# Kernel tuning notes

Hardware: AMD Instinct MI355X
Metric: run time of the kernel (lower is better)

The kernel has to match this reference:

```python
import jax, jax.numpy as jnp
import numpy as np

NODE_DIM = 256
EDGE_DIM = 128
NODE_IN = 768 + 769 + 4 + 1 + 3  # 1545


def setup_inputs() -> dict:
    key = jax.random.key(0)
    ks = jax.random.split(key, 16)
    B, N, H, W, C = 8, 128, 128, 128, 768
    obj_feats = jax.random.normal(ks[0], (B, N, 769), dtype=jnp.float32)
    masks = jax.random.uniform(ks[1], (B, N, H, W), dtype=jnp.float32)
    features = jax.random.normal(ks[2], (B, C, H, W), dtype=jnp.float32)
    bboxes = jax.random.uniform(ks[3], (B, N, 4), dtype=jnp.float32)
    conf = jax.random.uniform(ks[4], (B, N), dtype=jnp.float32)
    depth = jax.random.uniform(ks[5], (B, 1, H, W), dtype=jnp.float32) + 0.1
    # near-identity pose so homogeneous divide is well-conditioned
    pose = jnp.eye(4, dtype=jnp.float32)[None] + 0.01 * jax.random.normal(ks[6], (B, 4, 4), dtype=jnp.float32)
    s = 0.02
    node_w1 = s * jax.random.normal(ks[7], (512, NODE_IN), dtype=jnp.float32)
    node_b1 = jnp.zeros((512,), dtype=jnp.float32)
    node_w2 = s * jax.random.normal(ks[8], (NODE_DIM, 512), dtype=jnp.float32)
    node_b2 = jnp.zeros((NODE_DIM,), dtype=jnp.float32)
    edge_w1 = s * jax.random.normal(ks[9], (256, 2 * NODE_DIM), dtype=jnp.float32)
    edge_b1 = jnp.zeros((256,), dtype=jnp.float32)
    edge_w2 = s * jax.random.normal(ks[10], (EDGE_DIM, 256), dtype=jnp.float32)
    edge_b2 = jnp.zeros((EDGE_DIM,), dtype=jnp.float32)
    return dict(obj_feats=obj_feats, masks=masks, features=features, bboxes=bboxes,
                conf=conf, depth=depth, pose=pose,
                node_w1=node_w1, node_b1=node_b1, node_w2=node_w2, node_b2=node_b2,
                edge_w1=edge_w1, edge_b1=edge_b1, edge_w2=edge_w2, edge_b2=edge_b2)


def _forward(obj_feats, masks, features, bboxes, conf, depth, pose,
             node_w1, node_b1, node_w2, node_b2,
             edge_w1, edge_b1, edge_w2, edge_b2):
    B, C, H, W = features.shape
    N = masks.shape[1]
    K = jnp.eye(3, dtype=features.dtype)  # self.intrinsics

    # --- mask pooling: normalized mask-weighted average of features ---
    feats_flat = features.reshape(B, C, H * W)                 # [B,C,HW]
    m_flat = masks.reshape(B, N, H * W)                        # [B,N,HW]
    m_norm = m_flat / (m_flat.sum(-1, keepdims=True) + 1e-6)
    pooled = jnp.einsum('bnh,bch->bnc', m_norm, feats_flat)    # [B,N,C]

    # --- positional encoding ---
    x1, y1, x2, y2 = bboxes[..., 0], bboxes[..., 1], bboxes[..., 2], bboxes[..., 3]
    pos_feat = jnp.stack([(x1 + x2) / 2, (y1 + y2) / 2, x2 - x1, y2 - y1], axis=-1)  # [B,N,4]

    # --- motion prior ---
    ys = jnp.arange(H, dtype=masks.dtype)
    xs = jnp.arange(W, dtype=masks.dtype)
    mask_sum = masks.sum((-1, -2)) + 1e-6                      # [B,N]
    cx = jnp.einsum('bnhw,w->bn', masks, xs) / mask_sum
    cy = jnp.einsum('bnhw,h->bn', masks, ys) / mask_sum
    cx_idx = jnp.clip(jnp.round(cx).astype(jnp.int32), 0, W - 1)
    cy_idx = jnp.clip(jnp.round(cy).astype(jnp.int32), 0, H - 1)
    b_idx = jnp.arange(B)[:, None]                             # [B,1]
    z = depth[b_idx, 0, cy_idx, cx_idx]                        # [B,N]
    X = (cx - K[0, 2]) * z / K[0, 0]
    Y = (cy - K[1, 2]) * z / K[1, 1]
    ones = jnp.ones_like(z)
    P_h = jnp.stack([X, Y, z, ones], axis=-1)                  # [B,N,4]
    P_next = jnp.einsum('bij,bnj->bni', pose, P_h)             # [B,N,4]
    motion = P_next[..., :3] / P_next[..., 3:]                 # [B,N,3]

    # --- node MLP ---
    node_input = jnp.concatenate([pooled, obj_feats, pos_feat, conf[..., None], motion], axis=-1)
    h = jax.nn.relu(node_input @ node_w1.T + node_b1)
    node_emb = h @ node_w2.T + node_b2                         # [B,N,node_dim]

    # --- edge MLP: cat([n_i, n_j]) @ W1 == n_i @ W1a + n_j @ W1b (avoid O(N^2 * 2D) cat) ---
    D = node_emb.shape[-1]
    w1a, w1b = edge_w1[:, :D], edge_w1[:, D:]
    hi = node_emb @ w1a.T                                      # [B,N,256]
    hj = node_emb @ w1b.T                                      # [B,N,256]
    he = jax.nn.relu(hi[:, :, None, :] + hj[:, None, :, :] + edge_b1)  # [B,N,N,256]
    edge_emb = he @ edge_w2.T + edge_b2                        # [B,N,N,edge_dim]

    # --- adjacency: exp(-cdist) ---
    sq = jnp.sum(node_emb * node_emb, axis=-1)                 # [B,N]
    d2 = sq[:, :, None] + sq[:, None, :] - 2.0 * jnp.einsum('bnd,bmd->bnm', node_emb, node_emb)
    d2 = jnp.maximum(d2, 0.0)
    d = jnp.where(d2 > 0, jnp.sqrt(jnp.where(d2 > 0, d2, 1.0)), 0.0)  # grad-safe sqrt at 0
    adj = jnp.exp(-d)
    return node_emb, edge_emb, adj


def reference(obj_feats, masks, features, bboxes, conf, depth, pose,
              node_w1, node_b1, node_w2, node_b2,
              edge_w1, edge_b1, edge_w2, edge_b2):
    return _forward(obj_feats, masks, features, bboxes, conf, depth, pose,
                    node_w1, node_b1, node_w2, node_b2,
                    edge_w1, edge_b1, edge_w2, edge_b2)
```

## Files before the change

kernel.cpp:

```cpp
#include <hip/hip_runtime.h>
#include <hip/hip_bf16.h>

#define B_   8
#define N_   128
#define HW_  16384
#define C_   768
#define NIN_ 1545
#define NINP_ 1600
#define D1_  512
#define D_   256
#define EO_  128
#define KC_  8
#define CT_  12

typedef short s16x8 __attribute__((ext_vector_type(8)));
typedef float f32x16 __attribute__((ext_vector_type(16)));

__device__ __forceinline__ unsigned short f2bf(float x) {
  union { __hip_bfloat16 h; unsigned short u; } cv;
  cv.h = __float2bfloat16(x);
  return cv.u;
}

__global__ __launch_bounds__(256) void prep_k(const float* __restrict__ masks,
                                              const float* __restrict__ depth,
                                              const float* __restrict__ pose,
                                              float4* __restrict__ stats,
                                              unsigned short* __restrict__ masks_bf,
                                              const float* __restrict__ w1,
                                              const float* __restrict__ w2,
                                              const float* __restrict__ ew1,
                                              const float* __restrict__ ew2,
                                              unsigned short* __restrict__ w1b,
                                              unsigned short* __restrict__ w2b,
                                              unsigned short* __restrict__ we1b,
                                              unsigned short* __restrict__ ew2b) {
  if (blockIdx.x >= 1024) {
    int i = (blockIdx.x - 1024) * 256 + threadIdx.x;
    if (i < 512 * NINP_) {
      int r = i / NINP_, k = i - r * NINP_;
      w1b[i] = f2bf(k < NIN_ ? w1[r * NIN_ + k] : 0.0f);
      return;
    }
    i -= 512 * NINP_;
    if (i < 256 * 512) { w2b[i] = f2bf(w2[i]); return; }
    i -= 256 * 512;
    if (i < 512 * 256) {
      int r = i >> 8, k = i & 255;
      we1b[i] = f2bf(r < 256 ? ew1[r * 512 + k] : ew1[(r - 256) * 512 + 256 + k]);
      return;
    }
    i -= 512 * 256;
    if (i < 128 * 256) { ew2b[i] = f2bf(ew2[i]); }
    return;
  }
  int row = blockIdx.x;
  int b = row >> 7;
  const float4* mp = (const float4*)(masks + (size_t)row * HW_);
  unsigned short* mo = masks_bf + (size_t)row * HW_;
  double s = 0.0, sx = 0.0, sy = 0.0;
  for (int it = 0; it < 16; ++it) {
    int i4 = threadIdx.x + it * 256;
    float4 v = mp[i4];
    ushort4 pv = { f2bf(v.x), f2bf(v.y), f2bf(v.z), f2bf(v.w) };
    *(ushort4*)(mo + i4 * 4) = pv;
    int flat = i4 * 4;
    int y = flat >> 7, xb = flat & 127;
    double rs = (double)v.x + (double)v.y + (double)v.z + (double)v.w;
    s += rs;
    sx += (double)v.x * xb + (double)v.y * (xb + 1) + (double)v.z * (xb + 2) + (double)v.w * (xb + 3);
    sy += rs * (double)y;
  }
  for (int off = 32; off; off >>= 1) {
    s  += __shfl_down(s,  off);
    sx += __shfl_down(sx, off);
    sy += __shfl_down(sy, off);
  }
  __shared__ double red[3][4];
  int w = threadIdx.x >> 6, l = threadIdx.x & 63;
  if (l == 0) { red[0][w] = s; red[1][w] = sx; red[2][w] = sy; }
  __syncthreads();
  if (threadIdx.x == 0) {
    s  = red[0][0] + red[0][1] + red[0][2] + red[0][3];
    sx = red[1][0] + red[1][1] + red[1][2] + red[1][3];
    sy = red[2][0] + red[2][1] + red[2][2] + red[2][3];
    double msum = s + 1e-6;
    double cx = sx / msum, cy = sy / msum;
    int cxi = (int)rint(cx); cxi = min(127, max(0, cxi));
    int cyi = (int)rint(cy); cyi = min(127, max(0, cyi));
    double z = (double)depth[(size_t)b * HW_ + cyi * 128 + cxi];
    double Ph[4] = { cx * z, cy * z, z, 1.0 };
    const float* P = pose + b * 16;
    double pn[4];
    #pragma unroll
    for (int r = 0; r < 4; ++r)
      pn[r] = (double)P[r*4+0]*Ph[0] + (double)P[r*4+1]*Ph[1] + (double)P[r*4+2]*Ph[2] + (double)P[r*4+3]*Ph[3];
    double inv3 = 1.0 / pn[3];
    stats[row] = make_float4((float)(1.0 / msum), (float)(pn[0]*inv3), (float)(pn[1]*inv3), (float)(pn[2]*inv3));
  }
}

__global__ __launch_bounds__(256) void pooled_k(const unsigned short* __restrict__ masks_bf,
                                                const float* __restrict__ feats,
                                                float* __restrict__ Spart) {
  __shared__ short As[128 * 72];
  __shared__ short Bs[64 * 72];
  int id = blockIdx.x;
  int b  = id / 96;
  int lx = id - b * 96;
  int ct = lx % 12, kc = lx / 12;
  const unsigned short* mb = masks_bf + (size_t)b * N_ * HW_;
  const float* fb = feats + ((size_t)b * C_ + (size_t)ct * 64) * HW_;
  int t = threadIdx.x, w = t >> 6, l = t & 63;
  int rsel = l & 31, khalf = l >> 5;
  f32x16 acc[2];
  #pragma unroll
  for (int nt = 0; nt < 2; ++nt)
    #pragma unroll
    for (int i = 0; i < 16; ++i) acc[nt][i] = 0.0f;

  for (int kt = 0; kt < 32; ++kt) {
    int kbase = kc * 2048 + kt * 64;
    #pragma unroll
    for (int c = 0; c < 4; ++c) {
      int chunk = t + 256 * c;
      int row = chunk >> 3;
      int kof = (chunk & 7) * 8;
      *(uint4*)((unsigned short*)As + row * 72 + kof) =
          *(const uint4*)(mb + (size_t)row * HW_ + kbase + kof);
    }
    #pragma unroll
    for (int c = 0; c < 4; ++c) {
      int chunk = t + 256 * c;
      int row = chunk >> 4;
      int kof = (chunk & 15) << 2;
      float4 vb = *(const float4*)(fb + (size_t)row * HW_ + kbase + kof);
      ushort4 pb = { f2bf(vb.x), f2bf(vb.y), f2bf(vb.z), f2bf(vb.w) };
      *(ushort4*)((unsigned short*)Bs + row * 72 + kof) = pb;
    }
    __syncthreads();
    #pragma unroll
    for (int ks = 0; ks < 4; ++ks) {
      s16x8 a = *(const s16x8*)&As[(w * 32 + rsel) * 72 + ks * 16 + khalf * 8];
      #pragma unroll
      for (int nt = 0; nt < 2; ++nt) {
        s16x8 bf = *(const s16x8*)&Bs[(nt * 32 + rsel) * 72 + ks * 16 + khalf * 8];
        acc[nt] = __builtin_amdgcn_mfma_f32_32x32x16_bf16(a, bf, acc[nt], 0, 0, 0);
      }
    }
    __syncthreads();
  }
  float* op = Spart + (size_t)kc * 786432 + (size_t)b * 98304;
  #pragma unroll
  for (int nt = 0; nt < 2; ++nt)
    #pragma unroll
    for (int reg = 0; reg < 16; ++reg) {
      int rm = w * 32 + (reg & 3) + 8 * (reg >> 2) + 4 * khalf;
      int cn = ct * 64 + nt * 32 + rsel;
      op[rm * C_ + cn] = acc[nt][reg];
    }
}

__global__ __launch_bounds__(256) void assemble_k(const float* __restrict__ Spart,
                                                  const float4* __restrict__ stats,
                                                  const float* __restrict__ obj,
                                                  const float* __restrict__ bboxes,
                                                  const float* __restrict__ conf,
                                                  unsigned short* __restrict__ ni) {
  int r = blockIdx.x;
  float4 st = stats[r];
  float x1 = bboxes[r*4+0], y1 = bboxes[r*4+1], x2 = bboxes[r*4+2], y2 = bboxes[r*4+3];
  for (int k = threadIdx.x; k < NINP_; k += 256) {
    float v;
    if (k < 768) {
      float acc = 0.0f;
      #pragma unroll
      for (int kc = 0; kc < KC_; ++kc) acc += Spart[(size_t)kc * 786432 + (size_t)r * C_ + k];
      v = acc * st.x;
    } else if (k < 1537) v = obj[(size_t)r * 769 + (k - 768)];
    else if (k == 1537) v = 0.5f * (x1 + x2);
    else if (k == 1538) v = 0.5f * (y1 + y2);
    else if (k == 1539) v = x2 - x1;
    else if (k == 1540) v = y2 - y1;
    else if (k == 1541) v = conf[r];
    else if (k == 1542) v = st.y;
    else if (k == 1543) v = st.z;
    else if (k == 1544) v = st.w;
    else v = 0.0f;
    ni[(size_t)r * NINP_ + k] = f2bf(v);
  }
}

template <bool RELU, bool BIAS, int OUTM>
__global__ __launch_bounds__(256) void gemm64_k(const unsigned short* __restrict__ A,
                                                const unsigned short* __restrict__ Bm,
                                                const float* __restrict__ bias,
                                                float* __restrict__ Cf,
                                                unsigned short* __restrict__ Cb,
                                                int K, int N) {
  __shared__ short As[64 * 72];
  __shared__ short Bs[64 * 72];
  int n0 = blockIdx.x * 64, m0 = blockIdx.y * 64;
  int t = threadIdx.x, w = t >> 6, l = t & 63;
  int rsel = l & 31, khalf = l >> 5;
  int mh = (w & 1) * 32, nh = (w >> 1) * 32;
  f32x16 acc;
  #pragma unroll
  for (int i = 0; i < 16; ++i) acc[i] = 0.0f;

  for (int k0 = 0; k0 < K; k0 += 64) {
    #pragma unroll
    for (int c = 0; c < 2; ++c) {
      int chunk = t + 256 * c;
      int row = chunk >> 3, kof = (chunk & 7) * 8;
      *(uint4*)((unsigned short*)As + row * 72 + kof) =
          *(const uint4*)&A[(size_t)(m0 + row) * K + k0 + kof];
      *(uint4*)((unsigned short*)Bs + row * 72 + kof) =
          *(const uint4*)&Bm[(size_t)(n0 + row) * K + k0 + kof];
    }
    __syncthreads();
    #pragma unroll
    for (int ks = 0; ks < 4; ++ks) {
      s16x8 a = *(const s16x8*)&As[(mh + rsel) * 72 + ks * 16 + khalf * 8];
      s16x8 bf = *(const s16x8*)&Bs[(nh + rsel) * 72 + ks * 16 + khalf * 8];
      acc = __builtin_amdgcn_mfma_f32_32x32x16_bf16(a, bf, acc, 0, 0, 0);
    }
    __syncthreads();
  }
  #pragma unroll
  for (int reg = 0; reg < 16; ++reg) {
    int rm = m0 + mh + (reg & 3) + 8 * (reg >> 2) + 4 * khalf;
    int cn = n0 + nh + rsel;
    float v = acc[reg];
    if (BIAS) v += bias[cn];
    if (RELU) v = fmaxf(v, 0.0f);
    if (OUTM == 0 || OUTM == 2) Cf[(size_t)rm * N + cn] = v;
    if (OUTM == 1 || OUTM == 2) Cb[(size_t)rm * N + cn] = f2bf(v);
  }
}

__global__ __launch_bounds__(256) void edge_adj_k(const float* __restrict__ hihj,
                                                  const unsigned short* __restrict__ ew2b,
                                                  const float* __restrict__ eb1,
                                                  const float* __restrict__ eb2,
                                                  const float* __restrict__ ne,
                                                  float* __restrict__ out_edge,
                                                  float* __restrict__ out_adj) {
  __shared__ union {
    struct { short W2s[128 * 264]; float hi_s[256]; float b1_s[256]; float b2_s[128]; } e;
    struct { float njs[128 * 65]; float nei[256]; float red[3][256]; } a;
  } sm;
  int id = blockIdx.x;
  int lg = (id & 7) * 256 + (id >> 3);
  int t = threadIdx.x;

  if (lg < 1024) {
    int bi = lg;
    int b = bi >> 7;
    int w = t >> 6, l = t & 63;
    int rsel = l & 31, khalf = l >> 5;

    #pragma unroll
    for (int c = 0; c < 16; ++c) {
      int chunk = t + 256 * c;
      int row = chunk >> 5, kof = (chunk & 31) * 8;
      *(uint4*)((unsigned short*)sm.e.W2s + row * 264 + kof) = *(const uint4*)&ew2b[row * 256 + kof];
    }
    sm.e.hi_s[t] = hihj[(size_t)bi * 512 + t];
    sm.e.b1_s[t] = eb1[t];
    if (t < 128) sm.e.b2_s[t] = eb2[t];
    __syncthreads();

    f32x16 acc[4];
    #pragma unroll
    for (int nt = 0; nt < 4; ++nt)
      #pragma unroll
      for (int i = 0; i < 16; ++i) acc[nt][i] = 0.0f;

    const float* hjb = hihj + (size_t)b * 128 * 512 + 256;
    int jrow = w * 32 + rsel;
    #pragma unroll
    for (int ks = 0; ks < 16; ++ks) {
      int k0 = ks * 16 + khalf * 8;
      const float* hp = hjb + (size_t)jrow * 512 + k0;
      float4 h0 = *(const float4*)hp;
      float4 h1 = *(const float4*)(hp + 4);
      float f[8] = { h0.x, h0.y, h0.z, h0.w, h1.x, h1.y, h1.z, h1.w };
      s16x8 a;
      #pragma unroll
      for (int c = 0; c < 8; ++c)
        a[c] = (short)f2bf(fmaxf(f[c] + sm.e.hi_s[k0 + c] + sm.e.b1_s[k0 + c], 0.0f));
      #pragma unroll
      for (int nt = 0; nt < 4; ++nt) {
        s16x8 bf = *(const s16x8*)&sm.e.W2s[(nt * 32 + rsel) * 264 + k0];
        acc[nt] = __builtin_amdgcn_mfma_f32_32x32x16_bf16(a, bf, acc[nt], 0, 0, 0);
      }
    }
    float* ob = out_edge + (size_t)bi * 128 * 128;
    #pragma unroll
    for (int nt = 0; nt < 4; ++nt)
      #pragma unroll
      for (int reg = 0; reg < 16; ++reg) {
        int j = w * 32 + (reg & 3) + 8 * (reg >> 2) + 4 * khalf;
        int o = nt * 32 + rsel;
        ob[(size_t)j * 128 + o] = acc[nt][reg] + sm.e.b2_s[o];
      }
  } else {
    int bi = lg - 1024;
    int b = bi >> 7;
    const float* neb = ne + (size_t)b * 128 * 256;
    int j = t & 127, kh = t >> 7;
    sm.a.nei[t] = ne[(size_t)bi * 256 + t];
    float dot = 0.0f, sqj = 0.0f, sqi = 0.0f;
    for (int tile = 0; tile < 4; ++tile) {
      __syncthreads();
      #pragma unroll
      for (int p = 0; p < 8; ++p) {
        int f = p * 256 + t;
        int row = f >> 4;
        int k4 = (f & 15) << 2;
        float4 v = *(const float4*)(neb + (size_t)row * 256 + tile * 64 + k4);
        float* dst = &sm.a.njs[row * 65 + k4];
        dst[0] = v.x; dst[1] = v.y; dst[2] = v.z; dst[3] = v.w;
      }
      __syncthreads();
      int kb = tile * 64 + kh * 32;
      #pragma unroll
      for (int k = 0; k < 32; ++k) {
        float c = sm.a.njs[j * 65 + kh * 32 + k];
        float aa = sm.a.nei[kb + k];
        dot += aa * c; sqj += c * c; sqi += aa * aa;
      }
    }
    __syncthreads();
    sm.a.red[0][t] = dot; sm.a.red[1][t] = sqj; sm.a.red[2][t] = sqi;
    __syncthreads();
    if (t < 128) {
      dot = sm.a.red[0][t] + sm.a.red[0][t + 128];
      sqj = sm.a.red[1][t] + sm.a.red[1][t + 128];
      sqi = sm.a.red[2][t] + sm.a.red[2][t + 128];
      float d2 = fmaxf(sqi + sqj - 2.0f * dot, 0.0f);
      float d = d2 > 0.0f ? sqrtf(d2) : 0.0f;
      out_adj[(size_t)bi * 128 + t] = expf(-d);
    }
  }
}

extern "C" void kernel_launch(void* const* d_in, const int* in_sizes, int n_in,
                              void* d_out, int out_size, void* d_ws, size_t ws_size,
                              hipStream_t stream) {
  const float* obj    = (const float*)d_in[0];
  const float* masks  = (const float*)d_in[1];
  const float* feats  = (const float*)d_in[2];
  const float* bboxes = (const float*)d_in[3];
  const float* conf   = (const float*)d_in[4];
  const float* depth  = (const float*)d_in[5];
  const float* pose   = (const float*)d_in[6];
  const float* nw1    = (const float*)d_in[7];
  const float* nb1    = (const float*)d_in[8];
  const float* nw2    = (const float*)d_in[9];
  const float* nb2    = (const float*)d_in[10];
  const float* ew1    = (const float*)d_in[11];
  const float* eb1    = (const float*)d_in[12];
  const float* ew2    = (const float*)d_in[13];
  const float* eb2    = (const float*)d_in[14];

  char* ws = (char*)d_ws;
  float*          Spart = (float*)ws;
  unsigned short* h_bf  = (unsigned short*)ws;
  unsigned short* ne_bf = (unsigned short*)(ws + 1048576);
  float*          hihj  = (float*)(ws + 1572864);
  float4*         stats = (float4*)(ws + 25165824);
  unsigned short* ni_bf = (unsigned short*)(ws + 25182208);
  unsigned short* w1b   = (unsigned short*)(ws + 28459008);
  unsigned short* w2b   = (unsigned short*)(ws + 30097408);
  unsigned short* we1b  = (unsigned short*)(ws + 30359552);
  unsigned short* ew2b  = (unsigned short*)(ws + 30621696);
  unsigned short* mkbf  = (unsigned short*)(ws + 30687232);

  float* out      = (float*)d_out;
  float* out_ne   = out;
  float* out_edge = out + 262144;
  float* out_adj  = out + 262144 + 16777216;

  prep_k<<<dim3(5376), dim3(256), 0, stream>>>(masks, depth, pose, stats, mkbf,
                                               nw1, nw2, ew1, ew2, w1b, w2b, we1b, ew2b);
  pooled_k<<<dim3(768), dim3(256), 0, stream>>>(mkbf, feats, Spart);
  assemble_k<<<dim3(1024), dim3(256), 0, stream>>>(Spart, stats, obj, bboxes, conf, ni_bf);
  gemm64_k<true,  true,  1><<<dim3(8, 16), dim3(256), 0, stream>>>(ni_bf, w1b, nb1, nullptr, h_bf, NINP_, 512);
  gemm64_k<false, true,  2><<<dim3(4, 16), dim3(256), 0, stream>>>(h_bf, w2b, nb2, out_ne, ne_bf, 512, 256);
  gemm64_k<false, false, 0><<<dim3(8, 16), dim3(256), 0, stream>>>(ne_bf, we1b, nullptr, hihj, nullptr, 256, 512);
  edge_adj_k<<<dim3(2048), dim3(256), 0, stream>>>(hihj, ew2b, eb1, eb2, out_ne, out_edge, out_adj);
}
```

Before: 735.5 us.

## Fold edge W1 into node W2 to merge tail GEMMs and store hihj as bf16

Precomputes combo = edge_w1 · node_w2 and a folded bias so hi/hj come straight from the hidden activations. This lets the node-output GEMM and the hi/hj GEMM run as one launch (gemm23_k) instead of two dependent ones. It also moves the non-pooled node-input assembly into prep_k and stores hi/hj in bf16, which halves the edge kernel's reads. In exchange, prep_k does extra weight products, and reassociation plus bf16 rounding slightly change numerics.

```diff
diff --git a/kernel.cpp b/kernel.cpp
--- a/kernel.cpp
+++ b/kernel.cpp
@@ -11,9 +11,9 @@
 #define D_   256
 #define EO_  128
 #define KC_  8
-#define CT_  12
 
 typedef short s16x8 __attribute__((ext_vector_type(8)));
+typedef unsigned short u16x8 __attribute__((ext_vector_type(8)));
 typedef float f32x16 __attribute__((ext_vector_type(16)));
 
 __device__ __forceinline__ unsigned short f2bf(float x) {
@@ -21,22 +21,35 @@
   cv.h = __float2bfloat16(x);
   return cv.u;
 }
+__device__ __forceinline__ float bf2f(unsigned short u) {
+  union { unsigned int i; float f; } cv;
+  cv.i = ((unsigned int)u) << 16;
+  return cv.f;
+}
 
 __global__ __launch_bounds__(256) void prep_k(const float* __restrict__ masks,
                                               const float* __restrict__ depth,
                                               const float* __restrict__ pose,
+                                              const float* __restrict__ obj,
+                                              const float* __restrict__ bboxes,
+                                              const float* __restrict__ conf,
+                                              const float* __restrict__ nb2,
                                               float4* __restrict__ stats,
                                               unsigned short* __restrict__ masks_bf,
+                                              unsigned short* __restrict__ ni,
                                               const float* __restrict__ w1,
                                               const float* __restrict__ w2,
                                               const float* __restrict__ ew1,
                                               const float* __restrict__ ew2,
                                               unsigned short* __restrict__ w1b,
                                               unsigned short* __restrict__ w2b,
-                                              unsigned short* __restrict__ we1b,
-                                              unsigned short* __restrict__ ew2b) {
-  if (blockIdx.x >= 1024) {
-    int i = (blockIdx.x - 1024) * 256 + threadIdx.x;
+                                              unsigned short* __restrict__ ew2b,
+                                              unsigned short* __restrict__ combo_bf,
+                                              float* __restrict__ bc) {
+  int bid = blockIdx.x;
+  int t = threadIdx.x;
+  if (bid >= 1281) {
+    int i = (bid - 1281) * 256 + t;
     if (i < 512 * NINP_) {
       int r = i / NINP_, k = i - r * NINP_;
       w1b[i] = f2bf(k < NIN_ ? w1[r * NIN_ + k] : 0.0f);
@@ -45,22 +58,48 @@
     i -= 512 * NINP_;
     if (i < 256 * 512) { w2b[i] = f2bf(w2[i]); return; }
     i -= 256 * 512;
-    if (i < 512 * 256) {
-      int r = i >> 8, k = i & 255;
-      we1b[i] = f2bf(r < 256 ? ew1[r * 512 + k] : ew1[(r - 256) * 512 + 256 + k]);
-      return;
-    }
-    i -= 512 * 256;
     if (i < 128 * 256) { ew2b[i] = f2bf(ew2[i]); }
     return;
   }
-  int row = blockIdx.x;
+  if (bid == 1280) {
+    __shared__ float nb2s[256];
+    nb2s[t] = nb2[t];
+    __syncthreads();
+    for (int n = t; n < 512; n += 256) {
+      const float* er = (n < 256) ? &ew1[n * 512] : &ew1[(n - 256) * 512 + 256];
+      float acc = 0.0f;
+      for (int k2 = 0; k2 < 256; ++k2) acc += er[k2] * nb2s[k2];
+      bc[n] = acc;
+    }
+    return;
+  }
+  if (bid >= 1024) {
+    int cb = bid - 1024;
+    int n0 = cb * 2, n1 = n0 + 1;
+    __shared__ float wa[2][256];
+    wa[0][t] = (n0 < 256) ? ew1[n0 * 512 + t] : ew1[(n0 - 256) * 512 + 256 + t];
+    wa[1][t] = (n1 < 256) ? ew1[n1 * 512 + t] : ew1[(n1 - 256) * 512 + 256 + t];
+    __syncthreads();
+    float a00 = 0, a01 = 0, a10 = 0, a11 = 0;
+    for (int k2 = 0; k2 < 256; ++k2) {
+      float w0 = w2[k2 * 512 + t];
+      float w1v = w2[k2 * 512 + t + 256];
+      float e0 = wa[0][k2], e1 = wa[1][k2];
+      a00 += e0 * w0; a01 += e0 * w1v; a10 += e1 * w0; a11 += e1 * w1v;
+    }
+    combo_bf[n0 * 512 + t]       = f2bf(a00);
+    combo_bf[n0 * 512 + t + 256] = f2bf(a01);
+    combo_bf[n1 * 512 + t]       = f2bf(a10);
+    combo_bf[n1 * 512 + t + 256] = f2bf(a11);
+    return;
+  }
+  int row = bid;
   int b = row >> 7;
   const float4* mp = (const float4*)(masks + (size_t)row * HW_);
   unsigned short* mo = masks_bf + (size_t)row * HW_;
   double s = 0.0, sx = 0.0, sy = 0.0;
   for (int it = 0; it < 16; ++it) {
-    int i4 = threadIdx.x + it * 256;
+    int i4 = t + it * 256;
     float4 v = mp[i4];
     ushort4 pv = { f2bf(v.x), f2bf(v.y), f2bf(v.z), f2bf(v.w) };
     *(ushort4*)(mo + i4 * 4) = pv;
@@ -77,10 +116,11 @@
     sy += __shfl_down(sy, off);
   }
   __shared__ double red[3][4];
-  int w = threadIdx.x >> 6, l = threadIdx.x & 63;
+  __shared__ float4 sm_st;
+  int w = t >> 6, l = t & 63;
   if (l == 0) { red[0][w] = s; red[1][w] = sx; red[2][w] = sy; }
   __syncthreads();
-  if (threadIdx.x == 0) {
+  if (t == 0) {
     s  = red[0][0] + red[0][1] + red[0][2] + red[0][3];
     sx = red[1][0] + red[1][1] + red[1][2] + red[1][3];
     sy = red[2][0] + red[2][1] + red[2][2] + red[2][3];
@@ -96,7 +136,27 @@
     for (int r = 0; r < 4; ++r)
       pn[r] = (double)P[r*4+0]*Ph[0] + (double)P[r*4+1]*Ph[1] + (double)P[r*4+2]*Ph[2] + (double)P[r*4+3]*Ph[3];
     double inv3 = 1.0 / pn[3];
-    stats[row] = make_float4((float)(1.0 / msum), (float)(pn[0]*inv3), (float)(pn[1]*inv3), (float)(pn[2]*inv3));
+    float4 st = make_float4((float)(1.0 / msum), (float)(pn[0]*inv3), (float)(pn[1]*inv3), (float)(pn[2]*inv3));
+    stats[row] = st;
+    sm_st = st;
+  }
+  __syncthreads();
+  float4 st = sm_st;
+  float x1 = bboxes[row*4+0], y1 = bboxes[row*4+1], x2 = bboxes[row*4+2], y2 = bboxes[row*4+3];
+  unsigned short* nir = ni + (size_t)row * NINP_;
+  for (int k = 768 + t; k < NINP_; k += 256) {
+    float v;
+    if (k < 1537) v = obj[(size_t)row * 769 + (k - 768)];
+    else if (k == 1537) v = 0.5f * (x1 + x2);
+    else if (k == 1538) v = 0.5f * (y1 + y2);
+    else if (k == 1539) v = x2 - x1;
+    else if (k == 1540) v = y2 - y1;
+    else if (k == 1541) v = conf[row];
+    else if (k == 1542) v = st.y;
+    else if (k == 1543) v = st.z;
+    else if (k == 1544) v = st.w;
+    else v = 0.0f;
+    nir[k] = f2bf(v);
   }
 }
 
@@ -163,31 +223,14 @@
 
 __global__ __launch_bounds__(256) void assemble_k(const float* __restrict__ Spart,
                                                   const float4* __restrict__ stats,
-                                                  const float* __restrict__ obj,
-                                                  const float* __restrict__ bboxes,
-                                                  const float* __restrict__ conf,
                                                   unsigned short* __restrict__ ni) {
   int r = blockIdx.x;
-  float4 st = stats[r];
-  float x1 = bboxes[r*4+0], y1 = bboxes[r*4+1], x2 = bboxes[r*4+2], y2 = bboxes[r*4+3];
-  for (int k = threadIdx.x; k < NINP_; k += 256) {
-    float v;
-    if (k < 768) {
-      float acc = 0.0f;
-      #pragma unroll
-      for (int kc = 0; kc < KC_; ++kc) acc += Spart[(size_t)kc * 786432 + (size_t)r * C_ + k];
-      v = acc * st.x;
-    } else if (k < 1537) v = obj[(size_t)r * 769 + (k - 768)];
-    else if (k == 1537) v = 0.5f * (x1 + x2);
-    else if (k == 1538) v = 0.5f * (y1 + y2);
-    else if (k == 1539) v = x2 - x1;
-    else if (k == 1540) v = y2 - y1;
-    else if (k == 1541) v = conf[r];
-    else if (k == 1542) v = st.y;
-    else if (k == 1543) v = st.z;
-    else if (k == 1544) v = st.w;
-    else v = 0.0f;
-    ni[(size_t)r * NINP_ + k] = f2bf(v);
+  float sc = stats[r].x;
+  for (int k = threadIdx.x; k < 768; k += 256) {
+    float acc = 0.0f;
+    #pragma unroll
+    for (int kc = 0; kc < KC_; ++kc) acc += Spart[(size_t)kc * 786432 + (size_t)r * C_ + k];
+    ni[(size_t)r * NINP_ + k] = f2bf(acc * sc);
   }
 }
 
@@ -239,7 +282,56 @@
   }
 }
 
-__global__ __launch_bounds__(256) void edge_adj_k(const float* __restrict__ hihj,
+__global__ __launch_bounds__(256) void gemm23_k(const unsigned short* __restrict__ h_bf,
+                                                const unsigned short* __restrict__ w2b,
+                                                const unsigned short* __restrict__ combo_bf,
+                                                const float* __restrict__ nb2,
+                                                const float* __restrict__ bc,
+                                                float* __restrict__ out_ne,
+                                                unsigned short* __restrict__ hihj_bf) {
+  __shared__ short As[64 * 72];
+  __shared__ short Bs[64 * 72];
+  int bid = blockIdx.x;
+  const unsigned short* Bm; const float* bias; int N, n0, m0, mode;
+  if (bid < 64) { mode = 0; Bm = w2b;      bias = nb2; N = 256; n0 = (bid & 3) * 64; m0 = (bid >> 2) * 64; }
+  else { int i2 = bid - 64; mode = 1; Bm = combo_bf; bias = bc; N = 512; n0 = (i2 & 7) * 64; m0 = (i2 >> 3) * 64; }
+  int t = threadIdx.x, w = t >> 6, l = t & 63;
+  int rsel = l & 31, khalf = l >> 5;
+  int mh = (w & 1) * 32, nh = (w >> 1) * 32;
+  f32x16 acc;
+  #pragma unroll
+  for (int i = 0; i < 16; ++i) acc[i] = 0.0f;
+
+  for (int k0 = 0; k0 < 512; k0 += 64) {
+    #pragma unroll
+    for (int c = 0; c < 2; ++c) {
+      int chunk = t + 256 * c;
+      int row = chunk >> 3, kof = (chunk & 7) * 8;
+      *(uint4*)((unsigned short*)As + row * 72 + kof) =
+          *(const uint4*)&h_bf[(size_t)(m0 + row) * 512 + k0 + kof];
+      *(uint4*)((unsigned short*)Bs + row * 72 + kof) =
+          *(const uint4*)&Bm[(size_t)(n0 + row) * 512 + k0 + kof];
+    }
+    __syncthreads();
+    #pragma unroll
+    for (int ks = 0; ks < 4; ++ks) {
+      s16x8 a = *(const s16x8*)&As[(mh + rsel) * 72 + ks * 16 + khalf * 8];
+      s16x8 bf = *(const s16x8*)&Bs[(nh + rsel) * 72 + ks * 16 + khalf * 8];
+      acc = __builtin_amdgcn_mfma_f32_32x32x16_bf16(a, bf, acc, 0, 0, 0);
+    }
+    __syncthreads();
+  }
+  #pragma unroll
+  for (int reg = 0; reg < 16; ++reg) {
+    int rm = m0 + mh + (reg & 3) + 8 * (reg >> 2) + 4 * khalf;
+    int cn = n0 + nh + rsel;
+    float v = acc[reg] + bias[cn];
+    if (mode == 0) out_ne[(size_t)rm * 256 + cn] = v;
+    else           hihj_bf[(size_t)rm * 512 + cn] = f2bf(v);
+  }
+}
+
+__global__ __launch_bounds__(256) void edge_adj_k(const unsigned short* __restrict__ hihj_bf,
                                                   const unsigned short* __restrict__ ew2b,
                                                   const float* __restrict__ eb1,
                                                   const float* __restrict__ eb2,
@@ -247,7 +339,7 @@
                                                   float* __restrict__ out_edge,
                                                   float* __restrict__ out_adj) {
   __shared__ union {
-    struct { short W2s[128 * 264]; float hi_s[256]; float b1_s[256]; float b2_s[128]; } e;
+    struct { short W2s[128 * 264]; float hb_s[256]; float b2_s[128]; } e;
     struct { float njs[128 * 65]; float nei[256]; float red[3][256]; } a;
   } sm;
   int id = blockIdx.x;
@@ -266,8 +358,7 @@
       int row = chunk >> 5, kof = (chunk & 31) * 8;
       *(uint4*)((unsigned short*)sm.e.W2s + row * 264 + kof) = *(const uint4*)&ew2b[row * 256 + kof];
     }
-    sm.e.hi_s[t] = hihj[(size_t)bi * 512 + t];
-    sm.e.b1_s[t] = eb1[t];
+    sm.e.hb_s[t] = bf2f(hihj_bf[(size_t)bi * 512 + t]) + eb1[t];
     if (t < 128) sm.e.b2_s[t] = eb2[t];
     __syncthreads();
 
@@ -277,19 +368,16 @@
       #pragma unroll
       for (int i = 0; i < 16; ++i) acc[nt][i] = 0.0f;
 
-    const float* hjb = hihj + (size_t)b * 128 * 512 + 256;
+    const unsigned short* hjb = hihj_bf + (size_t)b * 128 * 512 + 256;
     int jrow = w * 32 + rsel;
     #pragma unroll
     for (int ks = 0; ks < 16; ++ks) {
       int k0 = ks * 16 + khalf * 8;
-      const float* hp = hjb + (size_t)jrow * 512 + k0;
-      float4 h0 = *(const float4*)hp;
-      float4 h1 = *(const float4*)(hp + 4);
-      float f[8] = { h0.x, h0.y, h0.z, h0.w, h1.x, h1.y, h1.z, h1.w };
+      u16x8 hv = *(const u16x8*)(hjb + (size_t)jrow * 512 + k0);
       s16x8 a;
       #pragma unroll
       for (int c = 0; c < 8; ++c)
-        a[c] = (short)f2bf(fmaxf(f[c] + sm.e.hi_s[k0 + c] + sm.e.b1_s[k0 + c], 0.0f));
+        a[c] = (short)f2bf(fmaxf(bf2f(hv[c]) + sm.e.hb_s[k0 + c], 0.0f));
       #pragma unroll
       for (int nt = 0; nt < 4; ++nt) {
         s16x8 bf = *(const s16x8*)&sm.e.W2s[(nt * 32 + rsel) * 264 + k0];
@@ -368,27 +456,28 @@
   char* ws = (char*)d_ws;
   float*          Spart = (float*)ws;
   unsigned short* h_bf  = (unsigned short*)ws;
-  unsigned short* ne_bf = (unsigned short*)(ws + 1048576);
-  float*          hihj  = (float*)(ws + 1572864);
+  unsigned short* hihjb = (unsigned short*)(ws + 1048576);
   float4*         stats = (float4*)(ws + 25165824);
   unsigned short* ni_bf = (unsigned short*)(ws + 25182208);
   unsigned short* w1b   = (unsigned short*)(ws + 28459008);
   unsigned short* w2b   = (unsigned short*)(ws + 30097408);
-  unsigned short* we1b  = (unsigned short*)(ws + 30359552);
-  unsigned short* ew2b  = (unsigned short*)(ws + 30621696);
-  unsigned short* mkbf  = (unsigned short*)(ws + 30687232);
+  unsigned short* ew2b  = (unsigned short*)(ws + 30359552);
+  unsigned short* combo = (unsigned short*)(ws + 30425088);
+  float*          bc    = (float*)(ws + 30949376);
+  unsigned short* mkbf  = (unsigned short*)(ws + 30951424);
 
   float* out      = (float*)d_out;
   float* out_ne   = out;
   float* out_edge = out + 262144;
   float* out_adj  = out + 262144 + 16777216;
 
-  prep_k<<<dim3(5376), dim3(256), 0, stream>>>(masks, depth, pose, stats, mkbf,
-                                               nw1, nw2, ew1, ew2, w1b, w2b, we1b, ew2b);
+  prep_k<<<dim3(5121), dim3(256), 0, stream>>>(masks, depth, pose, obj, bboxes, conf, nb2,
+                                               stats, mkbf, ni_bf,
+                                               nw1, nw2, ew1, ew2,
+                                               w1b, w2b, ew2b, combo, bc);
   pooled_k<<<dim3(768), dim3(256), 0, stream>>>(mkbf, feats, Spart);
-  assemble_k<<<dim3(1024), dim3(256), 0, stream>>>(Spart, stats, obj, bboxes, conf, ni_bf);
-  gemm64_k<true,  true,  1><<<dim3(8, 16), dim3(256), 0, stream>>>(ni_bf, w1b, nb1, nullptr, h_bf, NINP_, 512);
-  gemm64_k<false, true,  2><<<dim3(4, 16), dim3(256), 0, stream>>>(h_bf, w2b, nb2, out_ne, ne_bf, 512, 256);
-  gemm64_k<false, false, 0><<<dim3(8, 16), dim3(256), 0, stream>>>(ne_bf, we1b, nullptr, hihj, nullptr, 256, 512);
-  edge_adj_k<<<dim3(2048), dim3(256), 0, stream>>>(hihj, ew2b, eb1, eb2, out_ne, out_edge, out_adj);
-}
+  assemble_k<<<dim3(1024), dim3(256), 0, stream>>>(Spart, stats, ni_bf);
+  gemm64_k<true, true, 1><<<dim3(8, 16), dim3(256), 0, stream>>>(ni_bf, w1b, nb1, nullptr, h_bf, NINP_, 512);
+  gemm23_k<<<dim3(192), dim3(256), 0, stream>>>(h_bf, w2b, combo, nb2, bc, out_ne, hihjb);
+  edge_adj_k<<<dim3(2048), dim3(256), 0, stream>>>(hihjb, ew2b, eb1, eb2, out_ne, out_edge, out_adj);
+}
```

Result: no change. 743.3 us (+1.1%).
